# Kernel tuning notes

Measured on AMD Instinct MI355X. Metric: run time of the kernel, lower is better.

The kernel has to match this reference:

```python
import jax, jax.numpy as jnp
import numpy as np

B, S, D, H = 2, 2048, 1024, 16
DK = D // H  # 64


def setup_inputs() -> dict:
    key = jax.random.key(0)
    ks = jax.random.split(key, 9)
    w = lambda k_, shp: jax.random.normal(k_, shp, dtype=jnp.float32) * 0.02
    inp = {
        "q": jax.random.normal(ks[0], (B, S, D), dtype=jnp.float32),
        "k": jax.random.normal(ks[1], (B, S, D), dtype=jnp.float32),
        "v": jax.random.normal(ks[2], (B, S, D), dtype=jnp.float32),
        # causal mask, broadcastable over [B, H, S, S]; 0 -> masked
        "mask": jnp.tril(jnp.ones((S, S), dtype=jnp.int32))[None, None, :, :],
        "Wq": w(ks[3], (D, D)), "bq": w(ks[4], (D,)),
        "Wk": w(ks[5], (D, D)), "bk": w(ks[6], (D,)),
        "Wv": w(ks[7], (D, D)), "bv": w(ks[8], (D,)),
    }
    return inp


def _head_split(x):
    # [B, S, D] -> [B, H, S, DK]
    return x.reshape(B, S, H, DK).transpose(0, 2, 1, 3)


def reference(q, k, v, mask, Wq, bq, Wk, bk, Wv, bv):
    qh = _head_split(q @ Wq + bq)
    kh = _head_split(k @ Wk + bk)
    vh = _head_split(v @ Wv + bv)

    scores = jnp.einsum("bhqd,bhkd->bhqk", qh, kh) / jnp.sqrt(jnp.float32(DK))
    scores = jnp.where(mask == 0, -jnp.inf, scores)
    # original subtracts the GLOBAL max of the whole score tensor, then softmax
    scores = jax.nn.softmax(scores - jnp.max(scores), axis=-1)
    scores = jnp.where(jnp.isnan(scores), 0.0, scores)  # fully-masked rows -> 0

    out = jnp.einsum("bhqk,bhkd->bhqd", scores, vh)
    return out.transpose(0, 2, 1, 3).reshape(B, S, D)
```

## Files before the change

### kernel.cpp

```cpp
#include <hip/hip_runtime.h>
#include <hip/hip_bf16.h>
#include <stdint.h>

#define BB 2
#define SS 2048
#define DD 1024
#define HH 16
#define DKK 64

typedef __attribute__((ext_vector_type(8)))  __bf16 bfvec8;
typedef __attribute__((ext_vector_type(4)))  __bf16 bfvec4;
typedef __attribute__((ext_vector_type(4)))  float  f32x4;
typedef __attribute__((ext_vector_type(16))) float  f32x16;
typedef __attribute__((ext_vector_type(4)))  unsigned int u32x4;

__device__ __forceinline__ float exp2_fast(float x) {
    float r;
    asm("v_exp_f32 %0, %1" : "=v"(r) : "v"(x));
    return r;
}
__device__ __forceinline__ uint32_t cvt_pk(float lo, float hi) {
    uint32_t r;
    asm("v_cvt_pk_bf16_f32 %0, %1, %2" : "=v"(r) : "v"(lo), "v"(hi));
    return r;
}
__device__ __forceinline__ void plswap(uint32_t &x, uint32_t &y) {
    asm("v_permlane32_swap_b32 %0, %1" : "+v"(x), "+v"(y));
}
__device__ __forceinline__ f32x16 zero16() {
    return (f32x16){0.f,0.f,0.f,0.f,0.f,0.f,0.f,0.f,
                    0.f,0.f,0.f,0.f,0.f,0.f,0.f,0.f};
}
#define MFMA32(A, B, C) __builtin_amdgcn_mfma_f32_32x32x16_bf16((A), (B), (C), 0, 0, 0)

#define PACK(st, bofs, pa) do {                                   \
    uint32_t A1 = cvt_pk((st)[(bofs)+0], (st)[(bofs)+1]);         \
    uint32_t B1 = cvt_pk((st)[(bofs)+4], (st)[(bofs)+5]);         \
    uint32_t A2 = cvt_pk((st)[(bofs)+2], (st)[(bofs)+3]);         \
    uint32_t B2 = cvt_pk((st)[(bofs)+6], (st)[(bofs)+7]);         \
    plswap(A1, B1); plswap(A2, B2);                               \
    u32x4 u_; u_[0] = A1; u_[1] = A2; u_[2] = B1; u_[3] = B2;     \
    (pa) = __builtin_bit_cast(bfvec8, u_);                        \
} while (0)

__global__ void wt_kernel(const float* __restrict__ Wq, const float* __restrict__ Wk,
                          const float* __restrict__ Wv,
                          __bf16* __restrict__ Wtq, __bf16* __restrict__ Wtk,
                          __bf16* __restrict__ Wtv) {
    const float* W  = (blockIdx.z == 0) ? Wq  : (blockIdx.z == 1) ? Wk  : Wv;
    __bf16*      Wt = (blockIdx.z == 0) ? Wtq : (blockIdx.z == 1) ? Wtk : Wtv;
    __shared__ float tile[32][33];
    int k0 = blockIdx.x * 32;
    int n0 = blockIdx.y * 32;
    int tx = threadIdx.x, ty = threadIdx.y;
    for (int j = 0; j < 32; j += 8)
        tile[ty + j][tx] = W[(size_t)(k0 + ty + j) * DD + n0 + tx];
    __syncthreads();
    for (int j = 0; j < 32; j += 8)
        Wt[(size_t)(n0 + ty + j) * DD + k0 + tx] = (__bf16)tile[tx][ty + j];
}

#define BM 128
#define BN 128
#define BKP 64
#define LDA 72
#define LDV 68

__global__ __launch_bounds__(256)
void proj_kernel(const float* __restrict__ Xq, const float* __restrict__ Xk,
                 const float* __restrict__ Xv,
                 const __bf16* __restrict__ Wtq, const __bf16* __restrict__ Wtk,
                 const __bf16* __restrict__ Wtv,
                 const float* __restrict__ bq, const float* __restrict__ bk,
                 const float* __restrict__ bv,
                 __bf16* __restrict__ Qh, __bf16* __restrict__ Kh,
                 __bf16* __restrict__ VtG)
{
    int z = blockIdx.z;
    const float*  X    = (z == 0) ? Xq  : (z == 1) ? Xk  : Xv;
    const __bf16* Wt   = (z == 0) ? Wtq : (z == 1) ? Wtk : Wtv;
    const float*  bias = (z == 0) ? bq  : (z == 1) ? bk  : bv;
    const float scale  = (z == 0) ? 0.125f * 1.44269504088896340736f : 1.0f;

    __shared__ __align__(16) char praw[2 * BM * LDA * 2];
    __bf16* As = reinterpret_cast<__bf16*>(praw);
    __bf16* Bs = reinterpret_cast<__bf16*>(praw + BM * LDA * 2);

    int row_tile = blockIdx.x * 4 + (blockIdx.y >> 3);
    int col_tile = blockIdx.y & 7;
    int row0 = row_tile * BM;
    int col0 = col_tile * BN;

    int t    = threadIdx.x;
    int lane = t & 63;
    int w    = t >> 6;
    int wm   = w >> 1, wn = w & 1;
    int l15  = lane & 15;
    int hi   = lane >> 4;
    int kg   = hi * 8;

    f32x4 acc[4][4];
    for (int i = 0; i < 4; ++i)
        for (int j = 0; j < 4; ++j)
            acc[i][j] = (f32x4){0.f, 0.f, 0.f, 0.f};

    int rr = t >> 3;
    int c8 = (t & 7) * 8;

    f32x4 a0[4], a1[4];
    bfvec8 br[4];
    for (int i = 0; i < 4; ++i) {
        int row = rr + 32 * i;
        const float* xp = &X[(size_t)(row0 + row) * DD + c8];
        a0[i] = *reinterpret_cast<const f32x4*>(xp);
        a1[i] = *reinterpret_cast<const f32x4*>(xp + 4);
        br[i] = *reinterpret_cast<const bfvec8*>(
            &Wt[(size_t)(col0 + row) * DD + c8]);
    }

    #pragma unroll 2
    for (int k0 = 0; k0 < DD; k0 += BKP) {
        for (int i = 0; i < 4; ++i) {
            int row = rr + 32 * i;
            bfvec8 av;
            av[0] = (__bf16)a0[i][0]; av[1] = (__bf16)a0[i][1];
            av[2] = (__bf16)a0[i][2]; av[3] = (__bf16)a0[i][3];
            av[4] = (__bf16)a1[i][0]; av[5] = (__bf16)a1[i][1];
            av[6] = (__bf16)a1[i][2]; av[7] = (__bf16)a1[i][3];
            *reinterpret_cast<bfvec8*>(&As[row * LDA + c8]) = av;
            *reinterpret_cast<bfvec8*>(&Bs[row * LDA + c8]) = br[i];
        }

        bool more = (k0 + BKP) < DD;
        if (more) {
            int kn = k0 + BKP;
            for (int i = 0; i < 4; ++i) {
                int row = rr + 32 * i;
                const float* xp = &X[(size_t)(row0 + row) * DD + kn + c8];
                a0[i] = *reinterpret_cast<const f32x4*>(xp);
                a1[i] = *reinterpret_cast<const f32x4*>(xp + 4);
                br[i] = *reinterpret_cast<const bfvec8*>(
                    &Wt[(size_t)(col0 + row) * DD + kn + c8]);
            }
        }
        __syncthreads();

        for (int kk = 0; kk < BKP; kk += 32) {
            bfvec8 af[4], bf[4];
            for (int fm = 0; fm < 4; ++fm)
                af[fm] = *reinterpret_cast<const bfvec8*>(
                    &As[(wm * 64 + fm * 16 + l15) * LDA + kk + kg]);
            for (int fn = 0; fn < 4; ++fn)
                bf[fn] = *reinterpret_cast<const bfvec8*>(
                    &Bs[(wn * 64 + fn * 16 + l15) * LDA + kk + kg]);
            for (int fm = 0; fm < 4; ++fm)
                for (int fn = 0; fn < 4; ++fn)
                    acc[fm][fn] = __builtin_amdgcn_mfma_f32_16x16x32_bf16(
                        af[fm], bf[fn], acc[fm][fn], 0, 0, 0);
        }
        __syncthreads();
    }

    if (z != 2) {
        __bf16* Out = (z == 0) ? Qh : Kh;
        for (int fn = 0; fn < 4; ++fn) {
            int n  = col0 + wn * 64 + fn * 16 + l15;
            float bvl = bias[n];
            int h = n >> 6, dk = n & 63;
            for (int fm = 0; fm < 4; ++fm) {
                int mbase = row0 + wm * 64 + fm * 16 + hi * 4;
                for (int r = 0; r < 4; ++r) {
                    int m = mbase + r;
                    int b = m >> 11, s = m & 2047;
                    float v = (acc[fm][fn][r] + bvl) * scale;
                    Out[(((size_t)(b * HH + h) * SS) + s) * DKK + dk] = (__bf16)v;
                }
            }
        }
    } else {
        __bf16* tw = reinterpret_cast<__bf16*>(praw + w * (64 * LDV * 2));
        for (int fn = 0; fn < 4; ++fn) {
            int n  = col0 + wn * 64 + fn * 16 + l15;
            float bvl = bias[n];
            for (int fm = 0; fm < 4; ++fm) {
                int sl = fm * 16 + hi * 4;
                for (int r = 0; r < 4; ++r)
                    tw[(sl + r) * LDV + fn * 16 + l15] =
                        (__bf16)(acc[fm][fn][r] + bvl);
            }
        }
        int h  = (col0 + wn * 64) >> 6;
        int b  = row0 >> 11;
        int bh = b * HH + h;
        int sg = (row0 & 2047) + wm * 64;
        int d  = lane;
        __bf16* dst = VtG + ((size_t)bh * DKK + d) * SS + sg;
        for (int c = 0; c < 64; c += 8) {
            bfvec8 v;
            #pragma unroll
            for (int j = 0; j < 8; ++j)
                v[j] = tw[(c + j) * LDV + d];
            *reinterpret_cast<bfvec8*>(&dst[c]) = v;
        }
    }
}

#define QB 128
#define KB 64
#define LDK 72
#define NT (SS / QB)

__global__ __launch_bounds__(512, 4)
void attn_kernel(const __bf16* __restrict__ Qh, const __bf16* __restrict__ Kh,
                 const __bf16* __restrict__ VtG, float* __restrict__ out)
{
    __shared__ __align__(16) char ldsraw[36864 + 1024];
    __bf16* KsA = reinterpret_cast<__bf16*>(ldsraw);
    __bf16* KsB = reinterpret_cast<__bf16*>(ldsraw + 9216);
    __bf16* VsA = reinterpret_cast<__bf16*>(ldsraw + 18432);
    __bf16* VsB = reinterpret_cast<__bf16*>(ldsraw + 27648);
    float*  smc = reinterpret_cast<float*>(ldsraw + 36864);
    float*  mrg = reinterpret_cast<float*>(ldsraw);
    float*  ml  = reinterpret_cast<float*>(ldsraw + 32768);

    int bh = blockIdx.x;
    int qt = (NT - 1) - blockIdx.y;
    const size_t base = (size_t)bh * SS * DKK;
    const __bf16* Kb = Kh + base;
    const __bf16* Vb = VtG + base;

    int t    = threadIdx.x;
    int lane = t & 63;
    int w    = t >> 6;
    int rg   = w & 3;
    int half = w >> 2;
    int l31  = lane & 31;
    int hi2  = lane >> 5;

    int a    = qt * QB + rg * 32;
    int qrow = a + l31;

    const __bf16* ksb = half ? KsB : KsA;
    const __bf16* vsb = half ? VsB : VsA;

    bfvec8 qf0, qf1, qf2, qf3;
    {
        const __bf16* qp = &Qh[base + (size_t)qrow * DKK + hi2 * 8];
        qf0 = *reinterpret_cast<const bfvec8*>(qp);
        qf1 = *reinterpret_cast<const bfvec8*>(qp + 16);
        qf2 = *reinterpret_cast<const bfvec8*>(qp + 32);
        qf3 = *reinterpret_cast<const bfvec8*>(qp + 48);
    }

    f32x16 acc0 = zero16(), acc1 = zero16();
    float mrow = -1e30f, lrow = 0.f;

    int nkv   = (a + 31) / KB + 1;
    int pairs = qt + 1;

    int srow = t >> 3;
    int c8   = (t & 7) * 8;

    {
        bfvec8 ka = *reinterpret_cast<const bfvec8*>(&Kb[(size_t)srow * DKK + c8]);
        bfvec8 va = *reinterpret_cast<const bfvec8*>(&Vb[(size_t)srow * SS + c8]);
        bfvec8 kb = *reinterpret_cast<const bfvec8*>(&Kb[(size_t)(64 + srow) * DKK + c8]);
        bfvec8 vb = *reinterpret_cast<const bfvec8*>(&Vb[(size_t)srow * SS + 64 + c8]);
        *reinterpret_cast<bfvec8*>(&KsA[srow * LDK + c8]) = ka;
        *reinterpret_cast<bfvec8*>(&VsA[srow * LDK + c8]) = va;
        *reinterpret_cast<bfvec8*>(&KsB[srow * LDK + c8]) = kb;
        *reinterpret_cast<bfvec8*>(&VsB[srow * LDK + c8]) = vb;
    }
    __syncthreads();

    for (int j = 0; ; ++j) {
        bool more = (j + 1) < pairs;

        bfvec8 pkA, pvA, pkB, pvB;
        if (more) {
            int t0 = (2 * j + 2) * KB;
            pkA = *reinterpret_cast<const bfvec8*>(&Kb[(size_t)(t0 + srow) * DKK + c8]);
            pvA = *reinterpret_cast<const bfvec8*>(&Vb[(size_t)srow * SS + t0 + c8]);
            pkB = *reinterpret_cast<const bfvec8*>(&Kb[(size_t)(t0 + 64 + srow) * DKK + c8]);
            pvB = *reinterpret_cast<const bfvec8*>(&Vb[(size_t)srow * SS + t0 + 64 + c8]);
        }

        int tj = 2 * j + half;
        if (tj < nkv) {
            int kv64 = tj * KB;

            f32x16 st0 = zero16(), st1 = zero16();
            {
                int off = l31 * LDK + hi2 * 8;
                bfvec8 k0 = *reinterpret_cast<const bfvec8*>(&ksb[off]);
                bfvec8 k1 = *reinterpret_cast<const bfvec8*>(&ksb[off + 16]);
                bfvec8 k2 = *reinterpret_cast<const bfvec8*>(&ksb[off + 32]);
                bfvec8 k3 = *reinterpret_cast<const bfvec8*>(&ksb[off + 48]);
                st0 = MFMA32(k0, qf0, st0); st0 = MFMA32(k1, qf1, st0);
                st0 = MFMA32(k2, qf2, st0); st0 = MFMA32(k3, qf3, st0);
                int off1 = off + 32 * LDK;
                bfvec8 m0 = *reinterpret_cast<const bfvec8*>(&ksb[off1]);
                bfvec8 m1 = *reinterpret_cast<const bfvec8*>(&ksb[off1 + 16]);
                bfvec8 m2v = *reinterpret_cast<const bfvec8*>(&ksb[off1 + 32]);
                bfvec8 m3 = *reinterpret_cast<const bfvec8*>(&ksb[off1 + 48]);
                st1 = MFMA32(m0, qf0, st1); st1 = MFMA32(m1, qf1, st1);
                st1 = MFMA32(m2v, qf2, st1); st1 = MFMA32(m3, qf3, st1);
            }

            if (kv64 + 63 > a) {
                #pragma unroll
                for (int r = 0; r < 16; ++r) {
                    int cr = ((r & 3) + 8 * (r >> 2)) + 4 * hi2;
                    st0[r] = (kv64 + cr      > qrow) ? -1e30f : st0[r];
                    st1[r] = (kv64 + 32 + cr > qrow) ? -1e30f : st1[r];
                }
            }

            float m2 = -1e30f;
            #pragma unroll
            for (int r = 0; r < 16; ++r) {
                m2 = fmaxf(m2, st0[r]);
                m2 = fmaxf(m2, st1[r]);
            }
            m2 = fmaxf(m2, __shfl_xor(m2, 32));

            float corr = 1.0f;
            if (!__all(m2 - mrow <= 8.0f)) {
                float mn = fmaxf(mrow, m2);
                corr = exp2_fast(mrow - mn);
                mrow = mn;
                smc[w * 32 + l31] = corr;
                #pragma unroll
                for (int r = 0; r < 16; ++r) {
                    float rc = smc[w * 32 + ((r & 3) + 8 * (r >> 2)) + 4 * hi2];
                    acc0[r] *= rc;
                    acc1[r] *= rc;
                }
            }

            float rs = 0.f;
            #pragma unroll
            for (int r = 0; r < 16; ++r) {
                float p0 = exp2_fast(st0[r] - mrow); st0[r] = p0;
                float p1 = exp2_fast(st1[r] - mrow); st1[r] = p1;
                rs += p0 + p1;
            }
            rs += __shfl_xor(rs, 32);
            lrow = lrow * corr + rs;

            bfvec8 pa0, pa1, pa2, pa3;
            PACK(st0, 0, pa0); PACK(st0, 8, pa1);
            PACK(st1, 0, pa2); PACK(st1, 8, pa3);

            __builtin_amdgcn_s_setprio(1);
            {
                int voff = l31 * LDK + hi2 * 8;
                bfvec8 v0 = *reinterpret_cast<const bfvec8*>(&vsb[voff]);
                bfvec8 v1 = *reinterpret_cast<const bfvec8*>(&vsb[voff + 16]);
                bfvec8 v2 = *reinterpret_cast<const bfvec8*>(&vsb[voff + 32]);
                bfvec8 v3 = *reinterpret_cast<const bfvec8*>(&vsb[voff + 48]);
                acc0 = MFMA32(pa0, v0, acc0); acc0 = MFMA32(pa1, v1, acc0);
                acc0 = MFMA32(pa2, v2, acc0); acc0 = MFMA32(pa3, v3, acc0);
                int voff1 = voff + 32 * LDK;
                bfvec8 u0 = *reinterpret_cast<const bfvec8*>(&vsb[voff1]);
                bfvec8 u1 = *reinterpret_cast<const bfvec8*>(&vsb[voff1 + 16]);
                bfvec8 u2 = *reinterpret_cast<const bfvec8*>(&vsb[voff1 + 32]);
                bfvec8 u3 = *reinterpret_cast<const bfvec8*>(&vsb[voff1 + 48]);
                acc1 = MFMA32(pa0, u0, acc1); acc1 = MFMA32(pa1, u1, acc1);
                acc1 = MFMA32(pa2, u2, acc1); acc1 = MFMA32(pa3, u3, acc1);
            }
            __builtin_amdgcn_s_setprio(0);
        }

        if (!more) break;
        __syncthreads();
        *reinterpret_cast<bfvec8*>(&KsA[srow * LDK + c8]) = pkA;
        *reinterpret_cast<bfvec8*>(&VsA[srow * LDK + c8]) = pvA;
        *reinterpret_cast<bfvec8*>(&KsB[srow * LDK + c8]) = pkB;
        *reinterpret_cast<bfvec8*>(&VsB[srow * LDK + c8]) = pvB;
        __syncthreads();
    }

    __syncthreads();
    if (half == 1) {
        float* dst = mrg + ((size_t)(rg * 64 + lane)) * 32;
        #pragma unroll
        for (int r = 0; r < 16; ++r) { dst[r] = acc0[r]; dst[16 + r] = acc1[r]; }
        if (hi2 == 0) {
            ml[rg * 32 + l31]       = mrow;
            ml[128 + rg * 32 + l31] = lrow;
        }
    }
    __syncthreads();
    if (half == 0) {
        float mU = ml[rg * 32 + l31];
        float lU = ml[128 + rg * 32 + l31];
        float mS = fmaxf(mrow, mU);
        float cL = exp2_fast(mrow - mS), cU = exp2_fast(mU - mS);
        float li = 1.0f / (lrow * cL + lU * cU);
        smc[rg * 32 + l31]       = cL * li;
        smc[(rg + 4) * 32 + l31] = cU * li;
        const float* src = mrg + ((size_t)(rg * 64 + lane)) * 32;
        int b = bh >> 4, h = bh & 15;
        #pragma unroll
        for (int r = 0; r < 16; ++r) {
            int cr = ((r & 3) + 8 * (r >> 2)) + 4 * hi2;
            float sA = smc[rg * 32 + cr];
            float sB = smc[(rg + 4) * 32 + cr];
            int sg = a + cr;
            size_t o = ((size_t)(b * SS + sg)) * DD + h * DKK + l31;
            out[o]      = acc0[r] * sA + src[r]      * sB;
            out[o + 32] = acc1[r] * sA + src[16 + r] * sB;
        }
    }
}

extern "C" void kernel_launch(void* const* d_in, const int* in_sizes, int n_in,
                              void* d_out, int out_size, void* d_ws, size_t ws_size,
                              hipStream_t stream)
{
    const float* q  = (const float*)d_in[0];
    const float* k  = (const float*)d_in[1];
    const float* v  = (const float*)d_in[2];
    const float* Wq = (const float*)d_in[4];
    const float* bq = (const float*)d_in[5];
    const float* Wk = (const float*)d_in[6];
    const float* bk = (const float*)d_in[7];
    const float* Wv = (const float*)d_in[8];
    const float* bv = (const float*)d_in[9];
    float* out = (float*)d_out;

    char* ws = (char*)d_ws;
    __bf16* Qh  = (__bf16*)(ws + (size_t)0);
    __bf16* Kh  = (__bf16*)(ws + (size_t)8  * 1024 * 1024);
    __bf16* VtG = (__bf16*)(ws + (size_t)24 * 1024 * 1024);
    __bf16* Wtq = (__bf16*)(ws + (size_t)32 * 1024 * 1024);
    __bf16* Wtk = (__bf16*)(ws + (size_t)34 * 1024 * 1024);
    __bf16* Wtv = (__bf16*)(ws + (size_t)36 * 1024 * 1024);

    wt_kernel<<<dim3(32, 32, 3), dim3(32, 8), 0, stream>>>(
        Wq, Wk, Wv, Wtq, Wtk, Wtv);

    proj_kernel<<<dim3(8, 32, 3), 256, 0, stream>>>(
        q, k, v, Wtq, Wtk, Wtv, bq, bk, bv, Qh, Kh, VtG);

    attn_kernel<<<dim3(32, NT), 512, 0, stream>>>(Qh, Kh, VtG, out);
}
```

Measured before the change: 97.90 us.

## Double-buffer attention K/V LDS tiles and retune projection GEMM sync and priority

```diff
diff --git a/kernel.cpp b/kernel.cpp
--- a/kernel.cpp
+++ b/kernel.cpp
@@ -130,6 +130,7 @@
             *reinterpret_cast<bfvec8*>(&As[row * LDA + c8]) = av;
             *reinterpret_cast<bfvec8*>(&Bs[row * LDA + c8]) = br[i];
         }
+        __syncthreads();
 
         bool more = (k0 + BKP) < DD;
         if (more) {
@@ -143,8 +144,8 @@
                     &Wt[(size_t)(col0 + row) * DD + kn + c8]);
             }
         }
-        __syncthreads();
-
+
+        __builtin_amdgcn_s_setprio(1);
         for (int kk = 0; kk < BKP; kk += 32) {
             bfvec8 af[4], bf[4];
             for (int fm = 0; fm < 4; ++fm)
@@ -158,6 +159,7 @@
                     acc[fm][fn] = __builtin_amdgcn_mfma_f32_16x16x32_bf16(
                         af[fm], bf[fn], acc[fm][fn], 0, 0, 0);
         }
+        __builtin_amdgcn_s_setprio(0);
         __syncthreads();
     }
 
@@ -210,16 +212,12 @@
 #define LDK 72
 #define NT (SS / QB)
 
-__global__ __launch_bounds__(512, 4)
+__global__ __launch_bounds__(512, 2)
 void attn_kernel(const __bf16* __restrict__ Qh, const __bf16* __restrict__ Kh,
                  const __bf16* __restrict__ VtG, float* __restrict__ out)
 {
-    __shared__ __align__(16) char ldsraw[36864 + 1024];
-    __bf16* KsA = reinterpret_cast<__bf16*>(ldsraw);
-    __bf16* KsB = reinterpret_cast<__bf16*>(ldsraw + 9216);
-    __bf16* VsA = reinterpret_cast<__bf16*>(ldsraw + 18432);
-    __bf16* VsB = reinterpret_cast<__bf16*>(ldsraw + 27648);
-    float*  smc = reinterpret_cast<float*>(ldsraw + 36864);
+    __shared__ __align__(16) char ldsraw[73728 + 1024];
+    float*  smc = reinterpret_cast<float*>(ldsraw + 73728);
     float*  mrg = reinterpret_cast<float*>(ldsraw);
     float*  ml  = reinterpret_cast<float*>(ldsraw + 32768);
 
@@ -240,8 +238,8 @@
     int a    = qt * QB + rg * 32;
     int qrow = a + l31;
 
-    const __bf16* ksb = half ? KsB : KsA;
-    const __bf16* vsb = half ? VsB : VsA;
+    int koffb = half ? 9216 : 0;
+    int voffb = 18432 + koffb;
 
     bfvec8 qf0, qf1, qf2, qf3;
     {
@@ -262,19 +260,25 @@
     int c8   = (t & 7) * 8;
 
     {
-        bfvec8 ka = *reinterpret_cast<const bfvec8*>(&Kb[(size_t)srow * DKK + c8]);
-        bfvec8 va = *reinterpret_cast<const bfvec8*>(&Vb[(size_t)srow * SS + c8]);
-        bfvec8 kb = *reinterpret_cast<const bfvec8*>(&Kb[(size_t)(64 + srow) * DKK + c8]);
-        bfvec8 vb = *reinterpret_cast<const bfvec8*>(&Vb[(size_t)srow * SS + 64 + c8]);
-        *reinterpret_cast<bfvec8*>(&KsA[srow * LDK + c8]) = ka;
-        *reinterpret_cast<bfvec8*>(&VsA[srow * LDK + c8]) = va;
-        *reinterpret_cast<bfvec8*>(&KsB[srow * LDK + c8]) = kb;
-        *reinterpret_cast<bfvec8*>(&VsB[srow * LDK + c8]) = vb;
+        __bf16* KsA0 = reinterpret_cast<__bf16*>(ldsraw);
+        __bf16* KsB0 = reinterpret_cast<__bf16*>(ldsraw + 9216);
+        __bf16* VsA0 = reinterpret_cast<__bf16*>(ldsraw + 18432);
+        __bf16* VsB0 = reinterpret_cast<__bf16*>(ldsraw + 27648);
+        *reinterpret_cast<bfvec8*>(&KsA0[srow * LDK + c8]) =
+            *reinterpret_cast<const bfvec8*>(&Kb[(size_t)srow * DKK + c8]);
+        *reinterpret_cast<bfvec8*>(&VsA0[srow * LDK + c8]) =
+            *reinterpret_cast<const bfvec8*>(&Vb[(size_t)srow * SS + c8]);
+        *reinterpret_cast<bfvec8*>(&KsB0[srow * LDK + c8]) =
+            *reinterpret_cast<const bfvec8*>(&Kb[(size_t)(64 + srow) * DKK + c8]);
+        *reinterpret_cast<bfvec8*>(&VsB0[srow * LDK + c8]) =
+            *reinterpret_cast<const bfvec8*>(&Vb[(size_t)srow * SS + 64 + c8]);
     }
     __syncthreads();
 
     for (int j = 0; ; ++j) {
+        int  p    = j & 1;
         bool more = (j + 1) < pairs;
+        const char* bufp = ldsraw + p * 36864;
 
         bfvec8 pkA, pvA, pkB, pvB;
         if (more) {
@@ -288,6 +292,8 @@
         int tj = 2 * j + half;
         if (tj < nkv) {
             int kv64 = tj * KB;
+            const __bf16* ksb = reinterpret_cast<const __bf16*>(bufp + koffb);
+            const __bf16* vsb = reinterpret_cast<const __bf16*>(bufp + voffb);
 
             f32x16 st0 = zero16(), st1 = zero16();
             {
@@ -352,7 +358,6 @@
             PACK(st0, 0, pa0); PACK(st0, 8, pa1);
             PACK(st1, 0, pa2); PACK(st1, 8, pa3);
 
-            __builtin_amdgcn_s_setprio(1);
             {
                 int voff = l31 * LDK + hi2 * 8;
                 bfvec8 v0 = *reinterpret_cast<const bfvec8*>(&vsb[voff]);
@@ -369,15 +374,20 @@
                 acc1 = MFMA32(pa0, u0, acc1); acc1 = MFMA32(pa1, u1, acc1);
                 acc1 = MFMA32(pa2, u2, acc1); acc1 = MFMA32(pa3, u3, acc1);
             }
-            __builtin_amdgcn_s_setprio(0);
         }
 
         if (!more) break;
-        __syncthreads();
-        *reinterpret_cast<bfvec8*>(&KsA[srow * LDK + c8]) = pkA;
-        *reinterpret_cast<bfvec8*>(&VsA[srow * LDK + c8]) = pvA;
-        *reinterpret_cast<bfvec8*>(&KsB[srow * LDK + c8]) = pkB;
-        *reinterpret_cast<bfvec8*>(&VsB[srow * LDK + c8]) = pvB;
+        {
+            char* bufn = ldsraw + (p ^ 1) * 36864;
+            __bf16* KsAn = reinterpret_cast<__bf16*>(bufn);
+            __bf16* KsBn = reinterpret_cast<__bf16*>(bufn + 9216);
+            __bf16* VsAn = reinterpret_cast<__bf16*>(bufn + 18432);
+            __bf16* VsBn = reinterpret_cast<__bf16*>(bufn + 27648);
+            *reinterpret_cast<bfvec8*>(&KsAn[srow * LDK + c8]) = pkA;
+            *reinterpret_cast<bfvec8*>(&VsAn[srow * LDK + c8]) = pvA;
+            *reinterpret_cast<bfvec8*>(&KsBn[srow * LDK + c8]) = pkB;
+            *reinterpret_cast<bfvec8*>(&VsBn[srow * LDK + c8]) = pvB;
+        }
         __syncthreads();
     }
 
```

Result: faster. 87.27 us (median of 2 runs) (-10.9%).
